# Optimization experiments

Measured on AMD Instinct MI355X. Metric: run time of the kernel, lower is better.

Reference implementation:

```python
import jax, jax.numpy as jnp
import numpy as np
import math


def setup_inputs() -> dict:
    key = jax.random.key(0)
    ks = jax.random.split(key, 5)
    B, S, H = 4, 2048, 512
    scale = 1.0 / math.sqrt(H)
    return {
        "input_seq_rep": jax.random.normal(ks[0], (B, S, H), dtype=jnp.float32),
        "Wk": jax.random.normal(ks[1], (H, H), dtype=jnp.float32) * scale,
        "bk": jax.random.normal(ks[2], (H,), dtype=jnp.float32) * 0.01,
        "Wq": jax.random.normal(ks[3], (H, H), dtype=jnp.float32) * scale,
        "bq": jax.random.normal(ks[4], (H,), dtype=jnp.float32) * 0.01,
        "k_mul": 64,
    }


def reference(input_seq_rep, Wk, bk, Wq, bq, k_mul):
    B, S, H = input_seq_rep.shape
    x = jax.nn.relu(input_seq_rep)
    # torch Linear: y = x @ W.T + b
    k = jnp.einsum("bsh,oh->bso", x, Wk) + bk  # key (also used as value)
    q = jnp.einsum("bsh,oh->bso", x, Wq) + bq

    # local causal band mask: max(0, i - k_mul) <= j <= i
    i = jnp.arange(S)[:, None]
    j = jnp.arange(S)[None, :]
    mask = (j >= jnp.maximum(i - k_mul, 0)) & (j <= i)  # [S, S] bool

    scores = jnp.einsum("bqh,bkh->bqk", q, k) / jnp.sqrt(jnp.asarray(H, q.dtype))
    scores = jnp.where(mask[None, :, :], scores, jnp.asarray(-1e9, scores.dtype))
    attn = jax.nn.softmax(scores, axis=-1)  # [B, S, S]
    out = jnp.einsum("bqk,bkh->bqh", attn, k)  # value == key
    return out, attn
```

## Files before the change

kernel.cpp:

```cpp
#include <hip/hip_runtime.h>
#include <hip/hip_bf16.h>
#include <float.h>
#include <math.h>


typedef __attribute__((ext_vector_type(4))) float f32x4;
typedef __attribute__((ext_vector_type(8))) short short8;
typedef __attribute__((ext_vector_type(4))) short short4v;

#define TM 128
#define TN 128
#define TK 64

#define QBLK 32
#define KW 128
#define SCP 132
#define PPAD 136

static __device__ __forceinline__ short f2bf(float f) {
    __hip_bfloat16 h = __float2bfloat16(f);
    return *reinterpret_cast<short*>(&h);
}

__global__ __launch_bounds__(256) void gemm_mfma_relu_bias_bf16(
    const float* __restrict__ A,
    const float* __restrict__ Wq, const float* __restrict__ bq, short* __restrict__ Cq,
    const float* __restrict__ Wk, const float* __restrict__ bk, short* __restrict__ Ck,
    short* __restrict__ CkT,
    int M, int N, int K, int sshift)
{
    const float* W    = blockIdx.z ? Wk : Wq;
    const float* bias = blockIdx.z ? bk : bq;
    short*       C    = blockIdx.z ? Ck : Cq;

    __shared__ __align__(16) short lds[TM * TN];
    short* As = lds;
    short* Bs = lds + TM * TK;

    const int tid  = threadIdx.x;
    const int lane = tid & 63;
    const int wave = tid >> 6;
    const int wr   = (wave >> 1) * 64;
    const int wc   = (wave & 1) * 64;
    const int m0   = blockIdx.x * TM;
    const int n0   = blockIdx.y * TN;

    const int lr = lane & 15;
    const int lk = (lane >> 4) * 8;

    f32x4 acc[4][4];
    #pragma unroll
    for (int m = 0; m < 4; ++m)
        #pragma unroll
        for (int n = 0; n < 4; ++n)
            #pragma unroll
            for (int r = 0; r < 4; ++r) acc[m][n][r] = 0.f;

    for (int k0 = 0; k0 < K; k0 += TK) {
        #pragma unroll
        for (int i = 0; i < 8; ++i) {
            int f   = tid + (i << 8);
            int row = f >> 4;
            int cq  = (f & 15) << 2;
            int sidx = row * TK + (cq ^ ((row & 7) << 3));
            float4 va = *(const float4*)&A[(size_t)(m0 + row) * K + k0 + cq];
            short4v sa;
            sa.x = f2bf(fmaxf(va.x, 0.f));
            sa.y = f2bf(fmaxf(va.y, 0.f));
            sa.z = f2bf(fmaxf(va.z, 0.f));
            sa.w = f2bf(fmaxf(va.w, 0.f));
            *(short4v*)&As[sidx] = sa;
            float4 vb = *(const float4*)&W[(size_t)(n0 + row) * K + k0 + cq];
            short4v sb;
            sb.x = f2bf(vb.x);
            sb.y = f2bf(vb.y);
            sb.z = f2bf(vb.z);
            sb.w = f2bf(vb.w);
            *(short4v*)&Bs[sidx] = sb;
        }
        __syncthreads();

        #pragma unroll
        for (int kk = 0; kk < 2; ++kk) {
            short8 af[4], bf[4];
            #pragma unroll
            for (int m = 0; m < 4; ++m) {
                int r = wr + m * 16 + lr;
                af[m] = *(const short8*)&As[r * TK + ((kk * 32 + lk) ^ ((r & 7) << 3))];
            }
            #pragma unroll
            for (int n = 0; n < 4; ++n) {
                int r = wc + n * 16 + lr;
                bf[n] = *(const short8*)&Bs[r * TK + ((kk * 32 + lk) ^ ((r & 7) << 3))];
            }
            #pragma unroll
            for (int m = 0; m < 4; ++m)
                #pragma unroll
                for (int n = 0; n < 4; ++n)
                    acc[m][n] = __builtin_amdgcn_mfma_f32_16x16x32_bf16(
                        af[m], bf[n], acc[m][n], 0, 0, 0);
        }
        __syncthreads();
    }

    float bv[4];
    #pragma unroll
    for (int n = 0; n < 4; ++n) bv[n] = bias[n0 + wc + n * 16 + lr];
    const int cr = (lane >> 4) * 4;

    #pragma unroll
    for (int m = 0; m < 4; ++m)
        #pragma unroll
        for (int n = 0; n < 4; ++n) {
            int col = wc + n * 16 + lr;
            #pragma unroll
            for (int r = 0; r < 4; ++r) {
                int row = wr + m * 16 + cr + r;
                lds[row * TN + (col ^ ((row & 7) << 3))] = f2bf(acc[m][n][r] + bv[n]);
            }
        }
    __syncthreads();
    #pragma unroll
    for (int i = 0; i < 8; ++i) {
        int idx = tid + (i << 8);
        int m = idx >> 4, n8 = (idx & 15) << 3;
        short8 v = *(const short8*)&lds[m * TN + (n8 ^ ((m & 7) << 3))];
        *(short8*)&C[(size_t)(m0 + m) * N + n0 + n8] = v;
    }

    if (blockIdx.z) {
        __syncthreads();
        #pragma unroll
        for (int m = 0; m < 4; ++m)
            #pragma unroll
            for (int n = 0; n < 4; ++n) {
                int col = wc + n * 16 + lr;
                #pragma unroll
                for (int r = 0; r < 4; ++r) {
                    int row = wr + m * 16 + cr + r;
                    lds[col * TM + (row ^ ((col & 7) << 3))] = f2bf(acc[m][n][r] + bv[n]);
                }
            }
        __syncthreads();
        const int smask = (1 << sshift) - 1;
        #pragma unroll
        for (int i = 0; i < 8; ++i) {
            int idx = tid + (i << 8);
            int n = idx >> 4, m8 = (idx & 15) << 3;
            short8 v = *(const short8*)&lds[n * TM + (m8 ^ ((n & 7) << 3))];
            int gm = m0 + m8;
            int gb = gm >> sshift, s = gm & smask;
            *(short8*)&CkT[((size_t)gb * N + (n0 + n)) * (size_t)(smask + 1) + s] = v;
        }
    }
}

__global__ __launch_bounds__(512) void band_attn_mfma(
    const short* __restrict__ qbf, const short* __restrict__ kbf,
    const short* __restrict__ kT, const int* __restrict__ kmul_p,
    float* __restrict__ out, float* __restrict__ attn,
    int S, int H, float scale)
{
    __shared__ float sc[QBLK][SCP];
    __shared__ short pl[QBLK][PPAD];

    int bx = blockIdx.x;
    int tile = bx;
    if ((gridDim.x & 7) == 0) {
        int chunk = gridDim.x >> 3;
        tile = (bx & 7) * chunk + (bx >> 3);
    }

    const int i0  = tile * QBLK;
    const int b   = blockIdx.y;
    const int tid = threadIdx.x;
    const int lane = tid & 63;
    const int w    = tid >> 6;
    const int km   = kmul_p[0];
    const int jbase = max(i0 - km, 0);

    const int lr = lane & 15;
    const int lk = (lane >> 4) * 8;
    const int fr = (lane >> 4) * 4;

    f32x4 sacc[2];
    #pragma unroll
    for (int m = 0; m < 2; ++m)
        #pragma unroll
        for (int r = 0; r < 4; ++r) sacc[m][r] = 0.f;

    const short* qb = qbf + ((size_t)b * S + i0) * H;
    const short* kb = kbf + ((size_t)b * S + jbase) * H;
    #pragma unroll
    for (int ks = 0; ks < 16; ++ks) {
        int hoff = ks * 32 + lk;
        short8 qa0 = *(const short8*)(qb + (size_t)lr * H + hoff);
        short8 qa1 = *(const short8*)(qb + (size_t)(lr + 16) * H + hoff);
        short8 kf  = *(const short8*)(kb + (size_t)(w * 16 + lr) * H + hoff);
        sacc[0] = __builtin_amdgcn_mfma_f32_16x16x32_bf16(qa0, kf, sacc[0], 0, 0, 0);
        sacc[1] = __builtin_amdgcn_mfma_f32_16x16x32_bf16(qa1, kf, sacc[1], 0, 0, 0);
    }

    {
        int key = w * 16 + lr;
        int kg  = jbase + key;
        #pragma unroll
        for (int m = 0; m < 2; ++m)
            #pragma unroll
            for (int r = 0; r < 4; ++r) {
                int q = m * 16 + fr + r;
                int irow = i0 + q;
                bool ok = (kg <= irow) && (kg + km >= irow);
                sc[q][key] = ok ? sacc[m][r] * scale : -1e30f;
            }
    }
    __syncthreads();

    {
        int r  = tid >> 4;
        int t  = tid & 15;
        float4 v[2];
        #pragma unroll
        for (int j = 0; j < 2; ++j)
            v[j] = *(const float4*)&sc[r][t * 8 + j * 4];
        float mx = -FLT_MAX;
        #pragma unroll
        for (int j = 0; j < 2; ++j)
            mx = fmaxf(mx, fmaxf(fmaxf(v[j].x, v[j].y), fmaxf(v[j].z, v[j].w)));
        mx = fmaxf(mx, __shfl_xor(mx, 1, 64));
        mx = fmaxf(mx, __shfl_xor(mx, 2, 64));
        mx = fmaxf(mx, __shfl_xor(mx, 4, 64));
        mx = fmaxf(mx, __shfl_xor(mx, 8, 64));
        float e[8], s = 0.f;
        #pragma unroll
        for (int j = 0; j < 2; ++j) {
            e[j*4+0] = __expf(v[j].x - mx);
            e[j*4+1] = __expf(v[j].y - mx);
            e[j*4+2] = __expf(v[j].z - mx);
            e[j*4+3] = __expf(v[j].w - mx);
            s += e[j*4+0] + e[j*4+1] + e[j*4+2] + e[j*4+3];
        }
        s += __shfl_xor(s, 1, 64);
        s += __shfl_xor(s, 2, 64);
        s += __shfl_xor(s, 4, 64);
        s += __shfl_xor(s, 8, 64);
        float inv = __frcp_rn(s);
        #pragma unroll
        for (int j = 0; j < 2; ++j) {
            float4 p;
            p.x = e[j*4+0] * inv; p.y = e[j*4+1] * inv;
            p.z = e[j*4+2] * inv; p.w = e[j*4+3] * inv;
            *(float4*)&sc[r][t * 8 + j * 4] = p;
            short4v pb;
            pb.x = f2bf(p.x); pb.y = f2bf(p.y);
            pb.z = f2bf(p.z); pb.w = f2bf(p.w);
            *(short4v*)&pl[r][t * 8 + j * 4] = pb;
        }
    }
    __syncthreads();

    float* abase = attn + ((size_t)b * S + i0) * (size_t)S;
    const int col = tid * 4;
    #pragma unroll 4
    for (int r = 0; r < QBLK; ++r) {
        f32x4 o;
        #pragma unroll
        for (int j = 0; j < 4; ++j) {
            int rel = col + j - jbase;
            o[j] = ((unsigned)rel < (unsigned)KW) ? sc[r][rel] : 0.f;
        }
        __builtin_nontemporal_store(o, (f32x4*)(abase + (size_t)r * S + col));
    }

    short8 pa[2][4];
    #pragma unroll
    for (int m = 0; m < 2; ++m)
        #pragma unroll
        for (int ks = 0; ks < 4; ++ks)
            pa[m][ks] = *(const short8*)&pl[m * 16 + lr][ks * 32 + lk];

    const short* ktb = kT + (size_t)b * H * S;
    float* obase = out + ((size_t)b * S + i0) * H;
    #pragma unroll
    for (int nf = 0; nf < 4; ++nf) {
        int h = w * 64 + nf * 16 + lr;
        f32x4 oacc[2];
        #pragma unroll
        for (int r = 0; r < 4; ++r) { oacc[0][r] = 0.f; oacc[1][r] = 0.f; }
        #pragma unroll
        for (int ks = 0; ks < 4; ++ks) {
            short8 kf = *(const short8*)(ktb + (size_t)h * S + jbase + ks * 32 + lk);
            oacc[0] = __builtin_amdgcn_mfma_f32_16x16x32_bf16(pa[0][ks], kf, oacc[0], 0, 0, 0);
            oacc[1] = __builtin_amdgcn_mfma_f32_16x16x32_bf16(pa[1][ks], kf, oacc[1], 0, 0, 0);
        }
        #pragma unroll
        for (int m = 0; m < 2; ++m)
            #pragma unroll
            for (int r = 0; r < 4; ++r) {
                int q = m * 16 + fr + r;
                __builtin_nontemporal_store(oacc[m][r], obase + (size_t)q * H + h);
            }
    }
}

extern "C" void kernel_launch(void* const* d_in, const int* in_sizes, int n_in,
                              void* d_out, int out_size, void* d_ws, size_t ws_size,
                              hipStream_t stream)
{
    const float* x  = (const float*)d_in[0];
    const float* Wk = (const float*)d_in[1];
    const float* bk = (const float*)d_in[2];
    const float* Wq = (const float*)d_in[3];
    const float* bq = (const float*)d_in[4];
    const int*   km = (const int*)d_in[5];

    const int H = in_sizes[2];
    const long long BS = (long long)in_sizes[0] / H;
    const long long S = ((long long)out_size - (long long)in_sizes[0]) / BS;
    const int B = (int)(BS / S);
    int sshift = 0;
    while ((1LL << sshift) < S) ++sshift;

    short* kT  = (short*)d_ws;
    short* qbf = kT + (size_t)B * H * S;
    short* kbf = qbf + (size_t)BS * H;

    dim3 gg((unsigned)(BS / TM), (unsigned)(H / TN), 2);
    gemm_mfma_relu_bias_bf16<<<gg, 256, 0, stream>>>(
        x, Wq, bq, qbf, Wk, bk, kbf, kT, (int)BS, H, H, sshift);

    float* outp  = (float*)d_out;
    float* attnp = outp + (size_t)BS * H;
    const float scale = 1.0f / sqrtf((float)H);

    dim3 ag((unsigned)(S / QBLK), (unsigned)B);
    band_attn_mfma<<<ag, 512, 0, stream>>>(qbf, kbf, kT, km, outp, attnp,
                                           (int)S, H, scale);
}
```

Baseline: 56.85 us.

## Halve query block and shrink key window for banded attention tiles

Reduces the query tile from 32 to 16 rows and the key window from 128 to 96. The window is now anchored at i0-(KW-QBLK) instead of i0-k_mul. This cuts wasted QK and PV MFMA work on masked keys and doubles the block count for better CU coverage. Only 6 of 8 waves compute scores, and softmax runs on the first 256 threads with 6 columns each. The PV product and output store now run before the attention-matrix store, and the fixed window silently assumes k_mul is at most 80.

```diff
diff --git a/kernel.cpp b/kernel.cpp
--- a/kernel.cpp
+++ b/kernel.cpp
@@ -12,10 +12,10 @@
 #define TN 128
 #define TK 64
 
-#define QBLK 32
-#define KW 128
-#define SCP 132
-#define PPAD 136
+#define QBLK 16
+#define KW 96
+#define SCP 100
+#define PPAD 104
 
 static __device__ __forceinline__ short f2bf(float f) {
     __hip_bfloat16 h = __float2bfloat16(f);
@@ -177,87 +177,91 @@
     const int lane = tid & 63;
     const int w    = tid >> 6;
     const int km   = kmul_p[0];
-    const int jbase = max(i0 - km, 0);
+    const int jbase = max(i0 - (KW - QBLK), 0);
 
     const int lr = lane & 15;
     const int lk = (lane >> 4) * 8;
     const int fr = (lane >> 4) * 4;
 
-    f32x4 sacc[2];
-    #pragma unroll
-    for (int m = 0; m < 2; ++m)
-        #pragma unroll
-        for (int r = 0; r < 4; ++r) sacc[m][r] = 0.f;
-
     const short* qb = qbf + ((size_t)b * S + i0) * H;
     const short* kb = kbf + ((size_t)b * S + jbase) * H;
-    #pragma unroll
-    for (int ks = 0; ks < 16; ++ks) {
-        int hoff = ks * 32 + lk;
-        short8 qa0 = *(const short8*)(qb + (size_t)lr * H + hoff);
-        short8 qa1 = *(const short8*)(qb + (size_t)(lr + 16) * H + hoff);
-        short8 kf  = *(const short8*)(kb + (size_t)(w * 16 + lr) * H + hoff);
-        sacc[0] = __builtin_amdgcn_mfma_f32_16x16x32_bf16(qa0, kf, sacc[0], 0, 0, 0);
-        sacc[1] = __builtin_amdgcn_mfma_f32_16x16x32_bf16(qa1, kf, sacc[1], 0, 0, 0);
-    }
-
-    {
+    if (w < 6) {
+        f32x4 sacc;
+        #pragma unroll
+        for (int r = 0; r < 4; ++r) sacc[r] = 0.f;
+        #pragma unroll
+        for (int ks = 0; ks < 16; ++ks) {
+            int hoff = ks * 32 + lk;
+            short8 qa = *(const short8*)(qb + (size_t)lr * H + hoff);
+            short8 kf = *(const short8*)(kb + (size_t)(w * 16 + lr) * H + hoff);
+            sacc = __builtin_amdgcn_mfma_f32_16x16x32_bf16(qa, kf, sacc, 0, 0, 0);
+        }
         int key = w * 16 + lr;
         int kg  = jbase + key;
         #pragma unroll
-        for (int m = 0; m < 2; ++m)
-            #pragma unroll
-            for (int r = 0; r < 4; ++r) {
-                int q = m * 16 + fr + r;
-                int irow = i0 + q;
-                bool ok = (kg <= irow) && (kg + km >= irow);
-                sc[q][key] = ok ? sacc[m][r] * scale : -1e30f;
-            }
+        for (int r = 0; r < 4; ++r) {
+            int q = fr + r;
+            int irow = i0 + q;
+            bool ok = (kg <= irow) && (kg + km >= irow);
+            sc[q][key] = ok ? sacc[r] * scale : -1e30f;
+        }
     }
     __syncthreads();
 
-    {
-        int r  = tid >> 4;
-        int t  = tid & 15;
-        float4 v[2];
-        #pragma unroll
-        for (int j = 0; j < 2; ++j)
-            v[j] = *(const float4*)&sc[r][t * 8 + j * 4];
+    if (tid < 256) {
+        int r = tid >> 4;
+        int t = tid & 15;
+        float v[6];
+        #pragma unroll
+        for (int c = 0; c < 6; ++c) v[c] = sc[r][t * 6 + c];
         float mx = -FLT_MAX;
         #pragma unroll
-        for (int j = 0; j < 2; ++j)
-            mx = fmaxf(mx, fmaxf(fmaxf(v[j].x, v[j].y), fmaxf(v[j].z, v[j].w)));
+        for (int c = 0; c < 6; ++c) mx = fmaxf(mx, v[c]);
         mx = fmaxf(mx, __shfl_xor(mx, 1, 64));
         mx = fmaxf(mx, __shfl_xor(mx, 2, 64));
         mx = fmaxf(mx, __shfl_xor(mx, 4, 64));
         mx = fmaxf(mx, __shfl_xor(mx, 8, 64));
-        float e[8], s = 0.f;
-        #pragma unroll
-        for (int j = 0; j < 2; ++j) {
-            e[j*4+0] = __expf(v[j].x - mx);
-            e[j*4+1] = __expf(v[j].y - mx);
-            e[j*4+2] = __expf(v[j].z - mx);
-            e[j*4+3] = __expf(v[j].w - mx);
-            s += e[j*4+0] + e[j*4+1] + e[j*4+2] + e[j*4+3];
-        }
+        float e[6], s = 0.f;
+        #pragma unroll
+        for (int c = 0; c < 6; ++c) { e[c] = __expf(v[c] - mx); s += e[c]; }
         s += __shfl_xor(s, 1, 64);
         s += __shfl_xor(s, 2, 64);
         s += __shfl_xor(s, 4, 64);
         s += __shfl_xor(s, 8, 64);
         float inv = __frcp_rn(s);
         #pragma unroll
-        for (int j = 0; j < 2; ++j) {
-            float4 p;
-            p.x = e[j*4+0] * inv; p.y = e[j*4+1] * inv;
-            p.z = e[j*4+2] * inv; p.w = e[j*4+3] * inv;
-            *(float4*)&sc[r][t * 8 + j * 4] = p;
-            short4v pb;
-            pb.x = f2bf(p.x); pb.y = f2bf(p.y);
-            pb.z = f2bf(p.z); pb.w = f2bf(p.w);
-            *(short4v*)&pl[r][t * 8 + j * 4] = pb;
+        for (int c = 0; c < 6; ++c) {
+            float p = e[c] * inv;
+            sc[r][t * 6 + c] = p;
+            pl[r][t * 6 + c] = f2bf(p);
         }
     }
     __syncthreads();
+
+    short8 pa[3];
+    #pragma unroll
+    for (int ks = 0; ks < 3; ++ks)
+        pa[ks] = *(const short8*)&pl[lr][ks * 32 + lk];
+
+    const short* ktb = kT + (size_t)b * H * S;
+    float* obase = out + ((size_t)b * S + i0) * H;
+    #pragma unroll
+    for (int nf = 0; nf < 4; ++nf) {
+        int h = w * 64 + nf * 16 + lr;
+        f32x4 oacc;
+        #pragma unroll
+        for (int r = 0; r < 4; ++r) oacc[r] = 0.f;
+        #pragma unroll
+        for (int ks = 0; ks < 3; ++ks) {
+            short8 kf = *(const short8*)(ktb + (size_t)h * S + jbase + ks * 32 + lk);
+            oacc = __builtin_amdgcn_mfma_f32_16x16x32_bf16(pa[ks], kf, oacc, 0, 0, 0);
+        }
+        #pragma unroll
+        for (int r = 0; r < 4; ++r) {
+            int q = fr + r;
+            __builtin_nontemporal_store(oacc[r], obase + (size_t)q * H + h);
+        }
+    }
 
     float* abase = attn + ((size_t)b * S + i0) * (size_t)S;
     const int col = tid * 4;
@@ -270,36 +274,6 @@
             o[j] = ((unsigned)rel < (unsigned)KW) ? sc[r][rel] : 0.f;
         }
         __builtin_nontemporal_store(o, (f32x4*)(abase + (size_t)r * S + col));
-    }
-
-    short8 pa[2][4];
-    #pragma unroll
-    for (int m = 0; m < 2; ++m)
-        #pragma unroll
-        for (int ks = 0; ks < 4; ++ks)
-            pa[m][ks] = *(const short8*)&pl[m * 16 + lr][ks * 32 + lk];
-
-    const short* ktb = kT + (size_t)b * H * S;
-    float* obase = out + ((size_t)b * S + i0) * H;
-    #pragma unroll
-    for (int nf = 0; nf < 4; ++nf) {
-        int h = w * 64 + nf * 16 + lr;
-        f32x4 oacc[2];
-        #pragma unroll
-        for (int r = 0; r < 4; ++r) { oacc[0][r] = 0.f; oacc[1][r] = 0.f; }
-        #pragma unroll
-        for (int ks = 0; ks < 4; ++ks) {
-            short8 kf = *(const short8*)(ktb + (size_t)h * S + jbase + ks * 32 + lk);
-            oacc[0] = __builtin_amdgcn_mfma_f32_16x16x32_bf16(pa[0][ks], kf, oacc[0], 0, 0, 0);
-            oacc[1] = __builtin_amdgcn_mfma_f32_16x16x32_bf16(pa[1][ks], kf, oacc[1], 0, 0, 0);
-        }
-        #pragma unroll
-        for (int m = 0; m < 2; ++m)
-            #pragma unroll
-            for (int r = 0; r < 4; ++r) {
-                int q = m * 16 + fr + r;
-                __builtin_nontemporal_store(oacc[m][r], obase + (size_t)q * H + h);
-            }
     }
 }
 
```

Result: no change. 56.19 us (-1.2%).
